# Performance work log

Hardware: AMD Instinct MI355X
Metric: run time of the kernel (lower is better)

## Reference

```python
import jax, jax.numpy as jnp
import numpy as np

N_NODES = 50000


def gcn_conv(x, edge_index, W, b):
    """PyG GCNConv: add self-loops, sym-normalize, out = A_hat @ (x W) + b."""
    src, dst = edge_index[0], edge_index[1]
    n = x.shape[0]
    h = x @ W  # [N, out]
    # degree with self-loops (all edge weights = 1)
    deg = jax.ops.segment_sum(jnp.ones_like(dst, dtype=x.dtype), dst, num_segments=n) + 1.0
    dinv = jax.lax.rsqrt(deg)  # deg >= 1 so safe
    norm = dinv[src] * dinv[dst]  # [E]
    msgs = h[src] * norm[:, None]  # gather + scale
    agg = jax.ops.segment_sum(msgs, dst, num_segments=n)  # scatter-add
    agg = agg + h * (dinv * dinv)[:, None]  # self-loop term: norm_ii = dinv_i^2
    return agg + b


def setup_inputs() -> dict:
    key = jax.random.key(0)
    k_x, k_e, k_w1, k_w2 = jax.random.split(key, 4)
    in_ch, hid, out_ch = 256, 128, 128
    x = jax.random.normal(k_x, (N_NODES, in_ch), dtype=jnp.float32)
    edge_index = jax.random.randint(k_e, (2, 1_600_000), 0, N_NODES, dtype=jnp.int32)
    # Glorot-style init like PyG GCNConv
    W1 = jax.random.normal(k_w1, (in_ch, hid), dtype=jnp.float32) * (1.0 / np.sqrt(in_ch))
    b1 = jnp.zeros((hid,), dtype=jnp.float32)
    W2 = jax.random.normal(k_w2, (hid, out_ch), dtype=jnp.float32) * (1.0 / np.sqrt(hid))
    b2 = jnp.zeros((out_ch,), dtype=jnp.float32)
    return {"x": x, "edge_index": edge_index, "W1": W1, "b1": b1, "W2": W2, "b2": b2}


def reference(x, edge_index, W1, b1, W2, b2):
    # layer 1: GCNConv -> ReLU (dropout is identity in eval mode)
    h = jax.nn.relu(gcn_conv(x, edge_index, W1, b1))
    # layer 2: GCNConv -> ReLU
    out = jax.nn.relu(gcn_conv(h, edge_index, W2, b2))
    return out
```

## Files before the change

### kernel.cpp

```cpp
#include <hip/hip_runtime.h>
#include <cstdint>
#include <cstddef>


#define ELL_STRIDE 64
#define BCAP 8192
#define OVF_CAP 1024
#define PART_T 2048

typedef __attribute__((ext_vector_type(8))) short bf16x8;
typedef __attribute__((ext_vector_type(4))) float floatx4;

__device__ __forceinline__ unsigned short f2bf(float f) {
  unsigned int u = __float_as_uint(f);
  unsigned int r = (u + 0x7fffu + ((u >> 16) & 1u)) >> 16;
  return (unsigned short)r;
}
__device__ __forceinline__ float2 bfpair(unsigned int p) {
  float2 r;
  r.x = __uint_as_float(p << 16);
  r.y = __uint_as_float(p & 0xffff0000u);
  return r;
}

__global__ __launch_bounds__(256) void k_cvt_w(const float* __restrict__ W1,
                                               const float* __restrict__ W2,
                                               unsigned short* __restrict__ WT1,
                                               unsigned short* __restrict__ WT2,
                                               int* __restrict__ cursor,
                                               int* __restrict__ ovf_cnt,
                                               unsigned short* __restrict__ hb,
                                               int N, int NB) {
  int i = blockIdx.x * 256 + threadIdx.x;
  if (i < NB) cursor[i] = 0;
  if (i == NB) *ovf_cnt = 0;
  if (i < 128) {
    int chunk = i >> 5, j = i & 31;
    hb[(size_t)chunk * (N + 1) * 32 + (size_t)N * 32 + j] = 0;
  }
  if (i < 128 * 256) {
    int n = i >> 8, k = i & 255;
    WT1[i] = f2bf(W1[k * 128 + n]);
  } else if (i < 128 * 256 + 128 * 128) {
    int j = i - 128 * 256;
    int n = j >> 7, k = j & 127;
    WT2[j] = f2bf(W2[k * 128 + n]);
  }
}

__global__ __launch_bounds__(256) void k_part(const int* __restrict__ src,
                                              const int* __restrict__ dst,
                                              int* __restrict__ cursor,
                                              unsigned int* __restrict__ part,
                                              int* __restrict__ ovf_cnt,
                                              int* __restrict__ ovf,
                                              int E, int NB) {
  __shared__ unsigned int stage1[PART_T];
  __shared__ unsigned int stage2[PART_T];
  __shared__ int hist[512];
  __shared__ int base_g[512];
  __shared__ int base_l[512];
  __shared__ int cl[512];
  __shared__ int sc[256];
  const int tid = threadIdx.x;
  const int e0 = blockIdx.x * PART_T;
  int valid = E - e0; if (valid > PART_T) valid = PART_T;

  hist[tid] = 0; hist[tid + 256] = 0;
  cl[tid] = 0; cl[tid + 256] = 0;
  __syncthreads();
  for (int i = tid; i < valid; i += 256) {
    int e = e0 + i;
    unsigned int v = (unsigned int)(src[e] & 0xffff) | ((unsigned int)dst[e] << 16);
    stage1[i] = v;
    atomicAdd(&hist[(v >> 16) >> 7], 1);
  }
  __syncthreads();
  for (int b = tid; b < NB; b += 256) base_g[b] = atomicAdd(&cursor[b], hist[b]);
  int h0 = hist[2 * tid], h1 = hist[2 * tid + 1];
  int pv = h0 + h1;
  sc[tid] = pv;
  __syncthreads();
  #pragma unroll
  for (int off = 1; off < 256; off <<= 1) {
    int t = (tid >= off) ? sc[tid - off] : 0;
    __syncthreads();
    sc[tid] += t;
    __syncthreads();
  }
  int excl = sc[tid] - pv;
  base_l[2 * tid] = excl;
  base_l[2 * tid + 1] = excl + h0;
  __syncthreads();
  for (int i = tid; i < valid; i += 256) {
    unsigned int v = stage1[i];
    int b = (v >> 16) >> 7;
    int pos = base_l[b] + atomicAdd(&cl[b], 1);
    stage2[pos] = v;
  }
  __syncthreads();
  for (int i = tid; i < valid; i += 256) {
    unsigned int v = stage2[i];
    int b = (v >> 16) >> 7;
    int g = base_g[b] + (i - base_l[b]);
    if (g < BCAP) {
      part[(size_t)b * BCAP + g] = v;
    } else {
      int p = atomicAdd(ovf_cnt, 1);
      if (p < OVF_CAP) { ovf[2 * p] = (int)(v & 0xffffu); ovf[2 * p + 1] = (int)(v >> 16); }
    }
  }
}

__global__ __launch_bounds__(256) void k_fill2(const unsigned int* __restrict__ part,
                                               const int* __restrict__ cursor,
                                               unsigned short* __restrict__ col,
                                               int* __restrict__ cnt,
                                               float* __restrict__ dinv,
                                               int* __restrict__ ovf_cnt,
                                               int* __restrict__ ovf, int N) {
  __shared__ unsigned short slab[128 * ELL_STRIDE];
  __shared__ int cl[128];
  const int tid = threadIdx.x;
  const int b = blockIdx.x;
  if (tid < 128) cl[tid] = 0;
  {
    unsigned int dpk = ((unsigned int)N << 16) | (unsigned int)N;
    unsigned int* s32 = (unsigned int*)slab;
    #pragma unroll
    for (int i = 0; i < (128 * ELL_STRIDE / 2) / 256; ++i)
      s32[i * 256 + tid] = dpk;
  }
  __syncthreads();
  int count = cursor[b]; if (count > BCAP) count = BCAP;
  const unsigned int* p = part + (size_t)b * BCAP;
  for (int i = tid; i < count; i += 256) {
    unsigned int v = p[i];
    int row = (v >> 16) & 127;
    int k = atomicAdd(&cl[row], 1);
    if (k < ELL_STRIDE) {
      slab[row * ELL_STRIDE + k] = (unsigned short)(v & 0xffffu);
    } else {
      int q = atomicAdd(ovf_cnt, 1);
      if (q < OVF_CAP) { ovf[2 * q] = (int)(v & 0xffffu); ovf[2 * q + 1] = (int)(v >> 16); }
    }
  }
  __syncthreads();
  uint4* d4 = (uint4*)(col + (size_t)b * 128 * ELL_STRIDE);
  const uint4* s4 = (const uint4*)slab;
  #pragma unroll
  for (int i = 0; i < (128 * ELL_STRIDE * 2) / (16 * 256); ++i)
    d4[i * 256 + tid] = s4[i * 256 + tid];
  if (tid < 128) {
    int node = b * 128 + tid;
    if (node < N) {
      int c = cl[tid];
      cnt[node] = c;
      dinv[node] = rsqrtf((float)c + 1.0f);
    }
  }
}

template <int K, bool AF32>
__global__ __launch_bounds__(512) void k_gemm_mfma(const void* __restrict__ Xv,
                                                   const unsigned short* __restrict__ WT,
                                                   const float* __restrict__ dinv,
                                                   unsigned short* __restrict__ hb,
                                                   int M) {
  constexpr int KP = K + 8;
  __shared__ unsigned short Bs[128 * KP];
  const int tid = threadIdx.x;
  const int wave = tid >> 6, lane = tid & 63;
  const int q = lane >> 4, m = lane & 15;
  const int row0 = blockIdx.x * 128 + wave * 16;
  const bool active = row0 < M;
  const int arow = row0 + m;

  for (int c = tid; c < 128 * (K / 8); c += 512) {
    int r = c / (K / 8), ko = (c % (K / 8)) * 8;
    *(uint4*)(Bs + r * KP + ko) = *(const uint4*)(WT + (size_t)r * K + ko);
  }

  bf16x8 af[K / 32];
  if (active) {
    #pragma unroll
    for (int ks = 0; ks < K / 32; ++ks) {
      const int k0 = ks * 32 + q * 8;
      if (AF32) {
        const float* X = (const float*)Xv;
        float4 a0 = *(const float4*)(X + (size_t)arow * K + k0);
        float4 a1 = *(const float4*)(X + (size_t)arow * K + k0 + 4);
        af[ks] = (bf16x8){(short)f2bf(a0.x), (short)f2bf(a0.y),
                          (short)f2bf(a0.z), (short)f2bf(a0.w),
                          (short)f2bf(a1.x), (short)f2bf(a1.y),
                          (short)f2bf(a1.z), (short)f2bf(a1.w)};
      } else {
        af[ks] = *(const bf16x8*)((const unsigned short*)Xv +
                                  (size_t)arow * K + k0);
      }
    }
  }
  __syncthreads();
  if (!active) return;

  floatx4 acc[8];
  #pragma unroll
  for (int nt = 0; nt < 8; ++nt) acc[nt] = (floatx4){0.f, 0.f, 0.f, 0.f};
  #pragma unroll
  for (int ks = 0; ks < K / 32; ++ks) {
    const int k0 = ks * 32 + q * 8;
    #pragma unroll
    for (int nt = 0; nt < 8; ++nt) {
      bf16x8 bf = *(const bf16x8*)(Bs + (nt * 16 + m) * KP + k0);
      acc[nt] = __builtin_amdgcn_mfma_f32_16x16x32_bf16(af[ks], bf, acc[nt], 0, 0, 0);
    }
  }
  #pragma unroll
  for (int r = 0; r < 4; ++r) {
    int grow = row0 + q * 4 + r;
    float di = dinv[grow];
    #pragma unroll
    for (int nt = 0; nt < 8; ++nt)
      hb[(size_t)(nt >> 1) * (M + 1) * 32 + (size_t)grow * 32 + (nt & 1) * 16 + m] =
          f2bf(acc[nt][r] * di);
  }
}

template <bool BF16OUT>
__global__ __launch_bounds__(256) void k_agg(const uint4* __restrict__ hb4,
                                             const int* __restrict__ cnt,
                                             const unsigned short* __restrict__ col,
                                             const float* __restrict__ dinv,
                                             const int* __restrict__ ovf_cnt,
                                             const int* __restrict__ ovf,
                                             const float* __restrict__ bias,
                                             void* __restrict__ outv, int n) {
  __shared__ unsigned short cols[64][72];
  const int tid = threadIdx.x;
  const int chunk = blockIdx.x & 3;
  const int nd0 = (blockIdx.x >> 2) * 64;
  {
    unsigned int dpk = ((unsigned int)n << 16) | (unsigned int)n;
    int s = tid * 16;
    int node = s >> 6, off = s & 63;
    uint4 v0 = make_uint4(dpk, dpk, dpk, dpk), v1 = v0;
    if (nd0 + node < n) {
      v0 = *(const uint4*)(col + (size_t)(nd0 + node) * ELL_STRIDE + off);
      v1 = *(const uint4*)(col + (size_t)(nd0 + node) * ELL_STRIDE + off + 8);
    }
    *(uint4*)&cols[node][off] = v0;
    *(uint4*)&cols[node][off + 8] = v1;
  }
  __syncthreads();
  const int wave = tid >> 6, lane = tid & 63;
  const int nodeL = wave * 16 + (lane >> 2);
  const int q = lane & 3;
  const int d = nd0 + nodeL;
  const bool valid = d < n;
  const uint4* slab = hb4 + (size_t)chunk * (n + 1) * 4;
  const unsigned short* lc = cols[nodeL];

  float a0 = 0.f, a1 = 0.f, a2 = 0.f, a3 = 0.f;
  float a4 = 0.f, a5 = 0.f, a6 = 0.f, a7 = 0.f;
#define ADDP(P)                                                            \
  {                                                                        \
    float2 x0 = bfpair((P).x), x1 = bfpair((P).y);                         \
    float2 x2 = bfpair((P).z), x3 = bfpair((P).w);                         \
    a0 += x0.x; a1 += x0.y; a2 += x1.x; a3 += x1.y;                        \
    a4 += x2.x; a5 += x2.y; a6 += x3.x; a7 += x3.y;                        \
  }
  if (valid) {
    uint4 p = slab[(size_t)d * 4 + q];
    ADDP(p)
  }
  int m = valid ? cnt[d] : 0; if (m > ELL_STRIDE) m = ELL_STRIDE;
  int mmax = m;
  #pragma unroll
  for (int s = 4; s < 64; s <<= 1) {
    int o = __shfl_xor(mmax, s);
    mmax = o > mmax ? o : mmax;
  }
  for (int k = 0; k < mmax; k += 8) {
    ushort4 ca = *(const ushort4*)(lc + k);
    ushort4 cb = *(const ushort4*)(lc + k + 4);
    uint4 p0 = slab[(size_t)ca.x * 4 + q];
    uint4 p1 = slab[(size_t)ca.y * 4 + q];
    uint4 p2 = slab[(size_t)ca.z * 4 + q];
    uint4 p3 = slab[(size_t)ca.w * 4 + q];
    uint4 p4 = slab[(size_t)cb.x * 4 + q];
    uint4 p5 = slab[(size_t)cb.y * 4 + q];
    uint4 p6 = slab[(size_t)cb.z * 4 + q];
    uint4 p7 = slab[(size_t)cb.w * 4 + q];
    ADDP(p0) ADDP(p1) ADDP(p2) ADDP(p3)
    ADDP(p4) ADDP(p5) ADDP(p6) ADDP(p7)
  }
  if (valid) {
    int V = *ovf_cnt; if (V > OVF_CAP) V = OVF_CAP;
    for (int j = 0; j < V; ++j) {
      if (ovf[2 * j + 1] == d) {
        uint4 p = slab[(size_t)ovf[2 * j] * 4 + q];
        ADDP(p)
      }
    }
  }
#undef ADDP
  if (!valid) return;
  float di = dinv[d];
  float4 b0 = *(const float4*)(bias + chunk * 32 + q * 8);
  float4 b1 = *(const float4*)(bias + chunk * 32 + q * 8 + 4);
  float r0 = fmaxf(di * a0 + b0.x, 0.f);
  float r1 = fmaxf(di * a1 + b0.y, 0.f);
  float r2 = fmaxf(di * a2 + b0.z, 0.f);
  float r3 = fmaxf(di * a3 + b0.w, 0.f);
  float r4 = fmaxf(di * a4 + b1.x, 0.f);
  float r5 = fmaxf(di * a5 + b1.y, 0.f);
  float r6 = fmaxf(di * a6 + b1.z, 0.f);
  float r7 = fmaxf(di * a7 + b1.w, 0.f);
  if (BF16OUT) {
    uint4 pk;
    pk.x = (unsigned int)f2bf(r0) | ((unsigned int)f2bf(r1) << 16);
    pk.y = (unsigned int)f2bf(r2) | ((unsigned int)f2bf(r3) << 16);
    pk.z = (unsigned int)f2bf(r4) | ((unsigned int)f2bf(r5) << 16);
    pk.w = (unsigned int)f2bf(r6) | ((unsigned int)f2bf(r7) << 16);
    ((uint4*)outv)[(size_t)d * 16 + chunk * 4 + q] = pk;
  } else {
    float* o = (float*)outv + (size_t)d * 128 + chunk * 32 + q * 8;
    *(float4*)o = make_float4(r0, r1, r2, r3);
    *(float4*)(o + 4) = make_float4(r4, r5, r6, r7);
  }
}

extern "C" void kernel_launch(void* const* d_in, const int* in_sizes, int n_in,
                              void* d_out, int out_size, void* d_ws, size_t ws_size,
                              hipStream_t stream) {
  const float* x  = (const float*)d_in[0];
  const int*   ei = (const int*)d_in[1];
  const float* W1 = (const float*)d_in[2];
  const float* b1 = (const float*)d_in[3];
  const float* W2 = (const float*)d_in[4];
  const float* b2 = (const float*)d_in[5];
  float* out = (float*)d_out;

  const int IN_CH = 256;
  const int N = in_sizes[0] / IN_CH;
  const int E = in_sizes[1] / 2;
  const int NB = (N + 127) >> 7;

  const int* src = ei;
  const int* dst = ei + E;

  char* ws = (char*)d_ws;
  size_t off = 0;
  auto carve = [&](size_t bytes) {
    void* p = ws + off;
    off += (bytes + 255) & ~(size_t)255;
    return p;
  };
  int*            cursor  = (int*)carve((size_t)NB * 4);
  int*            ovf_cnt = (int*)carve(4);
  int*            ovf     = (int*)carve((size_t)OVF_CAP * 2 * 4);
  int*            cnt     = (int*)carve((size_t)N * 4);
  float*          dinv    = (float*)carve((size_t)N * 4);
  unsigned short* col     = (unsigned short*)carve((size_t)N * ELL_STRIDE * 2);
  unsigned short* hb      = (unsigned short*)carve((size_t)(N + 1) * 256);
  unsigned short* WT1     = (unsigned short*)carve(128 * 256 * 2);
  unsigned short* WT2     = (unsigned short*)carve(128 * 128 * 2);
  char*           unionp  = (char*)carve((size_t)NB * BCAP * 4);
  unsigned int*   part    = (unsigned int*)unionp;
  unsigned short* aggbuf  = (unsigned short*)unionp;

  k_cvt_w<<<(128 * 256 + 128 * 128 + 255) / 256, 256, 0, stream>>>(
      W1, W2, WT1, WT2, cursor, ovf_cnt, hb, N, NB);
  k_part <<<(E + PART_T - 1) / PART_T, 256, 0, stream>>>(src, dst, cursor, part,
                                                         ovf_cnt, ovf, E, NB);
  k_fill2<<<NB, 256, 0, stream>>>(part, cursor, col, cnt, dinv, ovf_cnt, ovf, N);

  int gblocks = (N + 127) / 128;
  int ablocks = 4 * ((N + 63) / 64);
  k_gemm_mfma<256, true ><<<gblocks, 512, 0, stream>>>(x, WT1, dinv, hb, N);
  k_agg<true ><<<ablocks, 256, 0, stream>>>((const uint4*)hb, cnt, col, dinv,
                                            ovf_cnt, ovf, b1, aggbuf, N);
  k_gemm_mfma<128, false><<<gblocks, 512, 0, stream>>>(aggbuf, WT2, dinv, hb, N);
  k_agg<false><<<ablocks, 256, 0, stream>>>((const uint4*)hb, cnt, col, dinv,
                                            ovf_cnt, ovf, b2, out, N);
}
```

Baseline: 236.9 us.

## Sort ELL rows by degree within each 128-node bucket to cut wavefront divergence

Within each 128-node bucket, k_fill2 now counting-sorts rows by their in-degree and writes the ELL column slab, counts and a permutation array in sorted order. k_agg processes rows in that permuted order and maps results back through perm. Wavefronts then hold nodes of similar degree, so the shuffle-max loop bound wastes fewer iterations. This adds a small shared-memory scan and sort in k_fill2, plus an extra perm load and scattered output writes in k_agg.

```diff
diff --git a/kernel.cpp b/kernel.cpp
--- a/kernel.cpp
+++ b/kernel.cpp
@@ -117,13 +117,18 @@
                                                unsigned short* __restrict__ col,
                                                int* __restrict__ cnt,
                                                float* __restrict__ dinv,
+                                               unsigned short* __restrict__ perm,
                                                int* __restrict__ ovf_cnt,
                                                int* __restrict__ ovf, int N) {
   __shared__ unsigned short slab[128 * ELL_STRIDE];
   __shared__ int cl[128];
+  __shared__ int posOf[128];
+  __shared__ int sbin[65];
+  __shared__ int bcur[65];
   const int tid = threadIdx.x;
   const int b = blockIdx.x;
   if (tid < 128) cl[tid] = 0;
+  if (tid >= 128 && tid < 128 + 65) { sbin[tid - 128] = 0; bcur[tid - 128] = 0; }
   {
     unsigned int dpk = ((unsigned int)N << 16) | (unsigned int)N;
     unsigned int* s32 = (unsigned int*)slab;
@@ -146,17 +151,44 @@
     }
   }
   __syncthreads();
+  if (tid < 128) {
+    int dg = cl[tid]; if (dg > 64) dg = 64;
+    atomicAdd(&sbin[dg], 1);
+  }
+  __syncthreads();
+  #pragma unroll
+  for (int off2 = 1; off2 < 65; off2 <<= 1) {
+    int v = 0;
+    if (tid < 65 && tid >= off2) v = sbin[tid - off2];
+    __syncthreads();
+    if (tid < 65) sbin[tid] += v;
+    __syncthreads();
+  }
+  if (tid < 128) {
+    int dg = cl[tid]; if (dg > 64) dg = 64;
+    int base = dg ? sbin[dg - 1] : 0;
+    posOf[tid] = base + atomicAdd(&bcur[dg], 1);
+  }
+  __syncthreads();
   uint4* d4 = (uint4*)(col + (size_t)b * 128 * ELL_STRIDE);
   const uint4* s4 = (const uint4*)slab;
   #pragma unroll
-  for (int i = 0; i < (128 * ELL_STRIDE * 2) / (16 * 256); ++i)
-    d4[i * 256 + tid] = s4[i * 256 + tid];
+  for (int pidx = 0; pidx < 4; ++pidx) {
+    int row = pidx * 32 + (tid >> 3);
+    int u = tid & 7;
+    d4[(size_t)posOf[row] * 8 + u] = s4[row * 8 + u];
+  }
   if (tid < 128) {
     int node = b * 128 + tid;
+    int gp = b * 128 + posOf[tid];
     if (node < N) {
       int c = cl[tid];
-      cnt[node] = c;
+      cnt[gp] = c;
+      perm[gp] = (unsigned short)node;
       dinv[node] = rsqrtf((float)c + 1.0f);
+    } else {
+      cnt[gp] = 0;
+      perm[gp] = (unsigned short)N;
     }
   }
 }
@@ -231,6 +263,7 @@
                                              const int* __restrict__ cnt,
                                              const unsigned short* __restrict__ col,
                                              const float* __restrict__ dinv,
+                                             const unsigned short* __restrict__ perm,
                                              const int* __restrict__ ovf_cnt,
                                              const int* __restrict__ ovf,
                                              const float* __restrict__ bias,
@@ -240,14 +273,10 @@
   const int chunk = blockIdx.x & 3;
   const int nd0 = (blockIdx.x >> 2) * 64;
   {
-    unsigned int dpk = ((unsigned int)n << 16) | (unsigned int)n;
     int s = tid * 16;
     int node = s >> 6, off = s & 63;
-    uint4 v0 = make_uint4(dpk, dpk, dpk, dpk), v1 = v0;
-    if (nd0 + node < n) {
-      v0 = *(const uint4*)(col + (size_t)(nd0 + node) * ELL_STRIDE + off);
-      v1 = *(const uint4*)(col + (size_t)(nd0 + node) * ELL_STRIDE + off + 8);
-    }
+    uint4 v0 = *(const uint4*)(col + (size_t)(nd0 + node) * ELL_STRIDE + off);
+    uint4 v1 = *(const uint4*)(col + (size_t)(nd0 + node) * ELL_STRIDE + off + 8);
     *(uint4*)&cols[node][off] = v0;
     *(uint4*)&cols[node][off + 8] = v1;
   }
@@ -256,7 +285,8 @@
   const int nodeL = wave * 16 + (lane >> 2);
   const int q = lane & 3;
   const int d = nd0 + nodeL;
-  const bool valid = d < n;
+  const int pd = perm[d];
+  const bool valid = pd < n;
   const uint4* slab = hb4 + (size_t)chunk * (n + 1) * 4;
   const unsigned short* lc = cols[nodeL];
 
@@ -269,11 +299,11 @@
     a0 += x0.x; a1 += x0.y; a2 += x1.x; a3 += x1.y;                        \
     a4 += x2.x; a5 += x2.y; a6 += x3.x; a7 += x3.y;                        \
   }
-  if (valid) {
-    uint4 p = slab[(size_t)d * 4 + q];
+  {
+    uint4 p = slab[(size_t)pd * 4 + q];
     ADDP(p)
   }
-  int m = valid ? cnt[d] : 0; if (m > ELL_STRIDE) m = ELL_STRIDE;
+  int m = cnt[d]; if (m > ELL_STRIDE) m = ELL_STRIDE;
   int mmax = m;
   #pragma unroll
   for (int s = 4; s < 64; s <<= 1) {
@@ -297,7 +327,7 @@
   if (valid) {
     int V = *ovf_cnt; if (V > OVF_CAP) V = OVF_CAP;
     for (int j = 0; j < V; ++j) {
-      if (ovf[2 * j + 1] == d) {
+      if (ovf[2 * j + 1] == pd) {
         uint4 p = slab[(size_t)ovf[2 * j] * 4 + q];
         ADDP(p)
       }
@@ -305,7 +335,7 @@
   }
 #undef ADDP
   if (!valid) return;
-  float di = dinv[d];
+  float di = dinv[pd];
   float4 b0 = *(const float4*)(bias + chunk * 32 + q * 8);
   float4 b1 = *(const float4*)(bias + chunk * 32 + q * 8 + 4);
   float r0 = fmaxf(di * a0 + b0.x, 0.f);
@@ -322,9 +352,9 @@
     pk.y = (unsigned int)f2bf(r2) | ((unsigned int)f2bf(r3) << 16);
     pk.z = (unsigned int)f2bf(r4) | ((unsigned int)f2bf(r5) << 16);
     pk.w = (unsigned int)f2bf(r6) | ((unsigned int)f2bf(r7) << 16);
-    ((uint4*)outv)[(size_t)d * 16 + chunk * 4 + q] = pk;
+    ((uint4*)outv)[(size_t)pd * 16 + chunk * 4 + q] = pk;
   } else {
-    float* o = (float*)outv + (size_t)d * 128 + chunk * 32 + q * 8;
+    float* o = (float*)outv + (size_t)pd * 128 + chunk * 32 + q * 8;
     *(float4*)o = make_float4(r0, r1, r2, r3);
     *(float4*)(o + 4) = make_float4(r4, r5, r6, r7);
   }
@@ -359,9 +389,10 @@
   int*            cursor  = (int*)carve((size_t)NB * 4);
   int*            ovf_cnt = (int*)carve(4);
   int*            ovf     = (int*)carve((size_t)OVF_CAP * 2 * 4);
-  int*            cnt     = (int*)carve((size_t)N * 4);
+  int*            cnt     = (int*)carve((size_t)NB * 128 * 4);
   float*          dinv    = (float*)carve((size_t)N * 4);
-  unsigned short* col     = (unsigned short*)carve((size_t)N * ELL_STRIDE * 2);
+  unsigned short* perm    = (unsigned short*)carve((size_t)NB * 128 * 2);
+  unsigned short* col     = (unsigned short*)carve((size_t)NB * 128 * ELL_STRIDE * 2);
   unsigned short* hb      = (unsigned short*)carve((size_t)(N + 1) * 256);
   unsigned short* WT1     = (unsigned short*)carve(128 * 256 * 2);
   unsigned short* WT2     = (unsigned short*)carve(128 * 128 * 2);
@@ -373,14 +404,15 @@
       W1, W2, WT1, WT2, cursor, ovf_cnt, hb, N, NB);
   k_part <<<(E + PART_T - 1) / PART_T, 256, 0, stream>>>(src, dst, cursor, part,
                                                          ovf_cnt, ovf, E, NB);
-  k_fill2<<<NB, 256, 0, stream>>>(part, cursor, col, cnt, dinv, ovf_cnt, ovf, N);
+  k_fill2<<<NB, 256, 0, stream>>>(part, cursor, col, cnt, dinv, perm,
+                                  ovf_cnt, ovf, N);
 
   int gblocks = (N + 127) / 128;
   int ablocks = 4 * ((N + 63) / 64);
   k_gemm_mfma<256, true ><<<gblocks, 512, 0, stream>>>(x, WT1, dinv, hb, N);
   k_agg<true ><<<ablocks, 256, 0, stream>>>((const uint4*)hb, cnt, col, dinv,
-                                            ovf_cnt, ovf, b1, aggbuf, N);
+                                            perm, ovf_cnt, ovf, b1, aggbuf, N);
   k_gemm_mfma<128, false><<<gblocks, 512, 0, stream>>>(aggbuf, WT2, dinv, hb, N);
   k_agg<false><<<ablocks, 256, 0, stream>>>((const uint4*)hb, cnt, col, dinv,
-                                            ovf_cnt, ovf, b2, out, N);
-}
+                                            perm, ovf_cnt, ovf, b2, out, N);
+}
```

Result: no change. 241.3 us (+1.9%).
